# Kernel optimization log

Measured on AMD Instinct MI355X. Metric: run time of the kernel, lower is better.

The kernel has to match this reference:

```python
import jax, jax.numpy as jnp
import numpy as np

N = 100_000          # total nodes across batch
E = 3_200_000        # total edges
L = 64               # token sequence length per node
VOCAB = 6
EMBED = 16
HID = 16             # gcn_hidden
EDGE_FEAT = 5
EDGE_HID = 16
NUM_GRAPHS = 64
NODE_IN = EMBED + 1  # Hseq concat x_cov


def setup_inputs() -> dict:
    key = jax.random.key(0)
    ks = jax.random.split(key, 14)
    seq_tokens = jax.random.randint(ks[0], (N, L), 0, VOCAB, dtype=jnp.int32)
    x_cov = jax.random.normal(ks[1], (N, 1), dtype=jnp.float32)
    edge_index = jax.random.randint(ks[2], (2, E), 0, N, dtype=jnp.int32)
    edge_attr = jax.random.normal(ks[3], (E, EDGE_FEAT), dtype=jnp.float32)
    batch = jnp.sort(jax.random.randint(ks[4], (N,), 0, NUM_GRAPHS, dtype=jnp.int32))
    # parameters
    embed = jax.random.normal(ks[5], (VOCAB, EMBED), dtype=jnp.float32) * 0.1
    embed = embed.at[0].set(0.0)  # padding_idx=0
    w1 = jax.random.normal(ks[6], (NODE_IN, HID), dtype=jnp.float32) * (NODE_IN ** -0.5)
    b1 = jnp.zeros((HID,), jnp.float32)
    w2 = jax.random.normal(ks[7], (HID, HID), dtype=jnp.float32) * (HID ** -0.5)
    b2 = jnp.zeros((HID,), jnp.float32)
    we1 = jax.random.normal(ks[8], (2 * HID + EDGE_FEAT, EDGE_HID), dtype=jnp.float32) * ((2 * HID + EDGE_FEAT) ** -0.5)
    be1 = jnp.zeros((EDGE_HID,), jnp.float32)
    we2 = jax.random.normal(ks[9], (EDGE_HID, 1), dtype=jnp.float32) * (EDGE_HID ** -0.5)
    be2 = jnp.zeros((1,), jnp.float32)
    return dict(seq_tokens=seq_tokens, x_cov=x_cov, edge_index=edge_index,
                edge_attr=edge_attr, batch=batch, embed=embed,
                w1=w1, b1=b1, w2=w2, b2=b2, we1=we1, be1=be1, we2=we2, be2=be2)


def reference(seq_tokens, x_cov, edge_index, edge_attr, batch,
              embed, w1, b1, w2, b2, we1, be1, we2, be2):
    # --- encode_nodes: masked mean of token embeddings + covariate ---
    Emb = embed[seq_tokens]                                   # [N, L, EMBED]
    mask = (seq_tokens != 0).astype(jnp.float32)[..., None]   # [N, L, 1]
    lengths = jnp.maximum(mask.sum(axis=1), 1.0)              # [N, 1]
    Hseq = (Emb * mask).sum(axis=1) / lengths                 # [N, EMBED]
    X = jnp.concatenate([Hseq, x_cov], axis=1)                # [N, NODE_IN]

    # --- per-graph dense GCN, expressed as equivalent block-diagonal sparse MP ---
    src, dst = edge_index[0], edge_index[1]
    valid = (batch[src] == batch[dst]).astype(jnp.float32)    # within-graph edges only
    # row-sum degree: out-degree (valid edges) + self loop + eps, per torch code
    deg = jax.ops.segment_sum(valid, src, num_segments=N) + 1.0 + 1e-8
    dinv = deg ** -0.5                                        # [N]

    def gcn(H, W, b):
        M = H @ W + b                                         # [N, HID]
        msg = (valid * dinv[dst])[:, None] * M[dst]           # [E, HID]
        agg = jax.ops.segment_sum(msg, src, num_segments=N)   # scatter-add over src
        return jax.nn.relu(dinv[:, None] * (agg + dinv[:, None] * M))

    H = gcn(X, w1, b1)
    H = gcn(H, w2, b2)

    # --- edge MLP on gathered node pairs ---
    feats = jnp.concatenate([H[src], H[dst], edge_attr], axis=1)  # [E, 2*HID+5]
    h = jax.nn.relu(feats @ we1 + be1)
    logits = (h @ we2 + be2)[:, 0]                            # [E]
    return logits
```

## Files before the change

kernel.cpp:

```cpp
#include <hip/hip_runtime.h>
#include <hip/hip_bf16.h>
#include <hip/hip_fp16.h>

#define BS 256
#define BS3 256
#define NG 64
#define NMAX 2048
#define SEGCAP 4096
#define SUBN 16
#define SUBCAP 256

__device__ __forceinline__ uint4 pack8(const float* f) {
    union { uint4 u; __half2 h[4]; } v;
    v.h[0] = __floats2half2_rn(f[0], f[1]);
    v.h[1] = __floats2half2_rn(f[2], f[3]);
    v.h[2] = __floats2half2_rn(f[4], f[5]);
    v.h[3] = __floats2half2_rn(f[6], f[7]);
    return v.u;
}

__device__ __forceinline__ void unpack8(uint4 u, float* f) {
    const __half2* h = (const __half2*)&u;
    float2 t;
    t = __half22float2(h[0]); f[0] = t.x; f[1] = t.y;
    t = __half22float2(h[1]); f[2] = t.x; f[3] = t.y;
    t = __half22float2(h[2]); f[4] = t.x; f[5] = t.y;
    t = __half22float2(h[3]); f[6] = t.x; f[7] = t.y;
}

__global__ __launch_bounds__(BS) void encode_kernel(
        const int* __restrict__ seq,
        const float* __restrict__ xcov,
        const int* __restrict__ batch,
        const float* __restrict__ embed,
        const float* __restrict__ w1,
        const float* __restrict__ b1,
        float* __restrict__ M1,
        int* __restrict__ gcnt,
        int* __restrict__ bnd, int N) {
    __shared__ float sE[96];
    __shared__ float sW1[272];
    __shared__ float sB1[16];
    int tid = threadIdx.x;
    for (int i = tid; i < 96; i += BS) sE[i] = embed[i];
    for (int i = tid; i < 272; i += BS) sW1[i] = w1[i];
    if (tid < 16) sB1[tid] = b1[tid];
    __syncthreads();

    if (blockIdx.x == 0) {
        for (int i = tid; i < NG * 16; i += BS) gcnt[i] = 0;
    }

    int n = blockIdx.x * BS + tid;
    if (n >= N) return;

    int b = batch[n];
    if (n == 0) {
        for (int g = 0; g <= b; g++) bnd[g] = 0;
    } else {
        int pb = batch[n - 1];
        for (int g = pb + 1; g <= b; g++) bnd[g] = n;
    }
    if (n == N - 1) {
        for (int g = b + 1; g <= NG; g++) bnd[g] = N;
    }

    const int4* t4 = (const int4*)(seq + (size_t)n * 64);
    int c1 = 0, c2 = 0, c3 = 0, c4 = 0, c5 = 0;
#pragma unroll
    for (int i = 0; i < 16; i++) {
        int4 v = t4[i];
        c1 += (v.x == 1) + (v.y == 1) + (v.z == 1) + (v.w == 1);
        c2 += (v.x == 2) + (v.y == 2) + (v.z == 2) + (v.w == 2);
        c3 += (v.x == 3) + (v.y == 3) + (v.z == 3) + (v.w == 3);
        c4 += (v.x == 4) + (v.y == 4) + (v.z == 4) + (v.w == 4);
        c5 += (v.x == 5) + (v.y == 5) + (v.z == 5) + (v.w == 5);
    }
    float f1 = (float)c1, f2 = (float)c2, f3 = (float)c3, f4 = (float)c4, f5 = (float)c5;
    float tot = f1 + f2 + f3 + f4 + f5;
    float inv = 1.0f / fmaxf(tot, 1.0f);
    float h[16];
#pragma unroll
    for (int j = 0; j < 16; j++)
        h[j] = (f1 * sE[16 + j] + f2 * sE[32 + j] + f3 * sE[48 + j] +
                f4 * sE[64 + j] + f5 * sE[80 + j]) * inv;
    float xc = xcov[n];
    float o[16];
#pragma unroll
    for (int j = 0; j < 16; j++) o[j] = sB1[j] + xc * sW1[256 + j];
#pragma unroll
    for (int k = 0; k < 16; k++) {
        float hk = h[k];
#pragma unroll
        for (int j = 0; j < 16; j++) o[j] += hk * sW1[k * 16 + j];
    }
    float4* mr = (float4*)(M1 + (size_t)n * 16);
    mr[0] = make_float4(o[0], o[1], o[2], o[3]);
    mr[1] = make_float4(o[4], o[5], o[6], o[7]);
    mr[2] = make_float4(o[8], o[9], o[10], o[11]);
    mr[3] = make_float4(o[12], o[13], o[14], o[15]);
}

__device__ __forceinline__ int find_graph(const int* bnd, int s) {
    int g = 0;
#pragma unroll
    for (int step = 32; step; step >>= 1) {
        int c = g + step;
        if (c <= NG - 1 && bnd[c] <= s) g = c;
    }
    return g;
}

__global__ __launch_bounds__(BS) void prep_kernel(
        const int* __restrict__ ei,
        const int* __restrict__ bndg,
        int2* __restrict__ glist,
        int* __restrict__ gcnt, int E) {
    __shared__ int sBnd[NG + 1];
    int tid = threadIdx.x;
    if (tid <= NG) sBnd[tid] = bndg[tid];
    __syncthreads();

    int sub = blockIdx.x & (SUBN - 1);
    int idx = (blockIdx.x * BS + tid) * 4;
    if (idx + 3 < E) {
        int4 s4 = *(const int4*)(ei + idx);
        int4 d4 = *(const int4*)(ei + E + idx);
#pragma unroll
        for (int j = 0; j < 4; j++) {
            int s = (&s4.x)[j], d = (&d4.x)[j];
            int g = find_graph(sBnd, s);
            if (d >= sBnd[g] && d < sBnd[g + 1]) {
                int pos = atomicAdd(&gcnt[g * 16 + sub], 1);
                if (pos < SUBCAP)
                    glist[(size_t)g * SEGCAP + sub * SUBCAP + pos] = make_int2(s, d);
            }
        }
    } else {
        for (int j = 0; j < 4; j++) {
            int e = idx + j;
            if (e < E) {
                int s = ei[e], d = ei[E + e];
                int g = find_graph(sBnd, s);
                if (d >= sBnd[g] && d < sBnd[g + 1]) {
                    int pos = atomicAdd(&gcnt[g * 16 + sub], 1);
                    if (pos < SUBCAP)
                        glist[(size_t)g * SEGCAP + sub * SUBCAP + pos] = make_int2(s, d);
                }
            }
        }
    }
}

__global__ __launch_bounds__(BS3) void csr_kernel(
        const int2* __restrict__ glist,
        const int* __restrict__ gcnt,
        const int* __restrict__ bnd,
        int2* __restrict__ OD,
        float* __restrict__ Dinv,
        int* __restrict__ csrD) {
    __shared__ int hist[NMAX];
    __shared__ int off[NMAX + 1];
    __shared__ int cur[NMAX];
    __shared__ int wsum[4];
    __shared__ int sCnt[SUBN];

    int tid = threadIdx.x;
    int g = blockIdx.x;
    int lo = bnd[g], hi = bnd[g + 1];
    int ng = hi - lo;
    if (ng > NMAX) ng = NMAX;

    for (int i = tid; i < NMAX; i += BS3) hist[i] = 0;
    if (tid < SUBN) {
        int c = gcnt[g * 16 + tid];
        sCnt[tid] = (c > SUBCAP) ? SUBCAP : c;
    }
    __syncthreads();

    if (ng <= 0) return;

    const int2* seg = glist + (size_t)g * SEGCAP;

    for (int idx = tid; idx < SUBN * SUBCAP; idx += BS3) {
        int c = idx >> 8;
        int k = idx & (SUBCAP - 1);
        if (k < sCnt[c]) atomicAdd(&hist[seg[c * SUBCAP + k].x - lo], 1);
    }
    __syncthreads();

    int i0 = tid * 8;
    int lv[8];
    int s = 0;
#pragma unroll
    for (int k = 0; k < 8; k++) { lv[k] = hist[i0 + k]; s += lv[k]; }
    int lane = tid & 63, wv = tid >> 6;
    int x = s;
#pragma unroll
    for (int o = 1; o < 64; o <<= 1) {
        int y = __shfl_up(x, o);
        if (lane >= o) x += y;
    }
    if (lane == 63) wsum[wv] = x;
    __syncthreads();
    if (wv == 0 && lane < 4) {
        int w = wsum[lane];
#pragma unroll
        for (int o = 1; o < 4; o <<= 1) {
            int y = __shfl_up(w, o);
            if (lane >= o) w += y;
        }
        wsum[lane] = w;
    }
    __syncthreads();
    int base = (wv > 0) ? wsum[wv - 1] : 0;
    int excl = base + x - s;
    int run = excl;
#pragma unroll
    for (int k = 0; k < 8; k++) {
        off[i0 + k] = run;
        cur[i0 + k] = run;
        run += lv[k];
    }
    __syncthreads();

    int gbase = g * SEGCAP;
    for (int i = tid; i < ng; i += BS3) {
        int beg = off[i];
        int dg = ((i + 1 < NMAX) ? off[i + 1] : beg) - beg;
        OD[lo + i] = make_int2(gbase + beg, dg);
        float dgf = (float)dg + 1.0f + 1e-8f;
        Dinv[lo + i] = 1.0f / sqrtf(dgf);
    }

    for (int idx = tid; idx < SUBN * SUBCAP; idx += BS3) {
        int c = idx >> 8;
        int k = idx & (SUBCAP - 1);
        if (k < sCnt[c]) {
            int2 e = seg[c * SUBCAP + k];
            int pos = atomicAdd(&cur[e.x - lo], 1);
            csrD[gbase + pos] = e.y;
        }
    }
}

__global__ __launch_bounds__(BS) void layer1_kernel(
        const int2* __restrict__ OD,
        const float* __restrict__ Dinv,
        const int* __restrict__ csrD,
        const float* __restrict__ M1,
        float* __restrict__ M2,
        const float* __restrict__ w2,
        const float* __restrict__ b2,
        int N) {
    __shared__ float sW2[256];
    __shared__ float sB2[16];
    int tid = threadIdx.x;
    for (int i = tid; i < 256; i += BS) sW2[i] = w2[i];
    if (tid < 16) sB2[tid] = b2[tid];
    __syncthreads();

    int n = blockIdx.x * BS + tid;
    if (n >= N) return;

    int2 od = OD[n];
    float di = Dinv[n];
    float acc[16];
#pragma unroll
    for (int j = 0; j < 16; j++) acc[j] = 0.f;
    int end = od.x + od.y;
    for (int e = od.x; e < end; e++) {
        int d = csrD[e];
        float dd = Dinv[d];
        const float4* m4 = (const float4*)(M1 + (size_t)d * 16);
        float4 a = m4[0], b = m4[1], c = m4[2], q = m4[3];
        acc[0] += dd * a.x; acc[1] += dd * a.y; acc[2] += dd * a.z; acc[3] += dd * a.w;
        acc[4] += dd * b.x; acc[5] += dd * b.y; acc[6] += dd * b.z; acc[7] += dd * b.w;
        acc[8] += dd * c.x; acc[9] += dd * c.y; acc[10] += dd * c.z; acc[11] += dd * c.w;
        acc[12] += dd * q.x; acc[13] += dd * q.y; acc[14] += dd * q.z; acc[15] += dd * q.w;
    }
    const float4* mr = (const float4*)(M1 + (size_t)n * 16);
    float4 m0 = mr[0], m1 = mr[1], m2 = mr[2], m3 = mr[3];
    float m[16] = {m0.x,m0.y,m0.z,m0.w, m1.x,m1.y,m1.z,m1.w,
                   m2.x,m2.y,m2.z,m2.w, m3.x,m3.y,m3.z,m3.w};
    float h[16];
#pragma unroll
    for (int j = 0; j < 16; j++) h[j] = fmaxf(di * (acc[j] + di * m[j]), 0.0f);
    float o[16];
#pragma unroll
    for (int j = 0; j < 16; j++) o[j] = sB2[j];
#pragma unroll
    for (int k = 0; k < 16; k++) {
        float hk = h[k];
#pragma unroll
        for (int j = 0; j < 16; j++) o[j] += hk * sW2[k * 16 + j];
    }
    float4* wr = (float4*)(M2 + (size_t)n * 16);
    wr[0] = make_float4(o[0], o[1], o[2], o[3]);
    wr[1] = make_float4(o[4], o[5], o[6], o[7]);
    wr[2] = make_float4(o[8], o[9], o[10], o[11]);
    wr[3] = make_float4(o[12], o[13], o[14], o[15]);
}

__global__ __launch_bounds__(BS) void layer2_kernel(
        const int2* __restrict__ OD,
        const float* __restrict__ Dinv,
        const int* __restrict__ csrD,
        const float* __restrict__ M2,
        char* __restrict__ PQ,
        const float* __restrict__ we1,
        int N) {
    __shared__ float sWe1[512];
    int tid = threadIdx.x;
    for (int i = tid; i < 512; i += BS) sWe1[i] = we1[i];
    __syncthreads();

    int n = blockIdx.x * BS + tid;
    if (n >= N) return;

    int2 od = OD[n];
    float di = Dinv[n];
    float acc[16];
#pragma unroll
    for (int j = 0; j < 16; j++) acc[j] = 0.f;
    int end = od.x + od.y;
    for (int e = od.x; e < end; e++) {
        int d = csrD[e];
        float dd = Dinv[d];
        const float4* m4 = (const float4*)(M2 + (size_t)d * 16);
        float4 a = m4[0], b = m4[1], c = m4[2], q = m4[3];
        acc[0] += dd * a.x; acc[1] += dd * a.y; acc[2] += dd * a.z; acc[3] += dd * a.w;
        acc[4] += dd * b.x; acc[5] += dd * b.y; acc[6] += dd * b.z; acc[7] += dd * b.w;
        acc[8] += dd * c.x; acc[9] += dd * c.y; acc[10] += dd * c.z; acc[11] += dd * c.w;
        acc[12] += dd * q.x; acc[13] += dd * q.y; acc[14] += dd * q.z; acc[15] += dd * q.w;
    }
    const float4* mr = (const float4*)(M2 + (size_t)n * 16);
    float4 m0 = mr[0], m1 = mr[1], m2 = mr[2], m3 = mr[3];
    float m[16] = {m0.x,m0.y,m0.z,m0.w, m1.x,m1.y,m1.z,m1.w,
                   m2.x,m2.y,m2.z,m2.w, m3.x,m3.y,m3.z,m3.w};
    float h[16];
#pragma unroll
    for (int j = 0; j < 16; j++) h[j] = fmaxf(di * (acc[j] + di * m[j]), 0.0f);
    float p[16], q[16];
#pragma unroll
    for (int j = 0; j < 16; j++) { p[j] = 0.f; q[j] = 0.f; }
#pragma unroll
    for (int k = 0; k < 16; k++) {
        float hk = h[k];
#pragma unroll
        for (int j = 0; j < 16; j++) {
            p[j] += hk * sWe1[k * 16 + j];
            q[j] += hk * sWe1[(16 + k) * 16 + j];
        }
    }
    uint4* pr = (uint4*)(PQ + (size_t)n * 64);
    pr[0] = pack8(p); pr[1] = pack8(p + 8);
    pr[2] = pack8(q); pr[3] = pack8(q + 8);
}

__global__ __launch_bounds__(BS) void edge_mlp_kernel(
        const int* __restrict__ ei,
        const char* __restrict__ PQ,
        const float* __restrict__ eattr,
        const float* __restrict__ we1,
        const float* __restrict__ be1,
        const float* __restrict__ we2,
        const float* __restrict__ be2,
        float* __restrict__ out, int E) {
    __shared__ float sC[80];
    __shared__ float sB[16];
    __shared__ float sV[16];
    __shared__ float sb2;
    int tid = threadIdx.x;
    if (tid < 80) sC[tid] = we1[512 + tid];
    if (tid < 16) { sB[tid] = be1[tid]; sV[tid] = we2[tid]; }
    if (tid == 0) sb2 = be2[0];
    __syncthreads();
    int e = blockIdx.x * BS + tid;
    if (e >= E) return;
    int s = __builtin_nontemporal_load(ei + e);
    int d = __builtin_nontemporal_load(ei + E + e);
    const uint4* pr = (const uint4*)(PQ + (size_t)s * 64);
    const uint4* qr = (const uint4*)(PQ + (size_t)d * 64 + 32);
    uint4 pa = pr[0], pb = pr[1];
    uint4 qa = qr[0], qb = qr[1];
    const float* ea = eattr + (size_t)e * 5;
    float a0 = __builtin_nontemporal_load(ea + 0);
    float a1 = __builtin_nontemporal_load(ea + 1);
    float a2 = __builtin_nontemporal_load(ea + 2);
    float a3 = __builtin_nontemporal_load(ea + 3);
    float a4 = __builtin_nontemporal_load(ea + 4);

    float p[16], q[16];
    unpack8(pa, p); unpack8(pb, p + 8);
    unpack8(qa, q); unpack8(qb, q + 8);

    float lg = sb2;
#pragma unroll
    for (int j = 0; j < 16; j++) {
        float acc = sB[j] + p[j] + q[j] +
                    a0 * sC[j] + a1 * sC[16 + j] + a2 * sC[32 + j] +
                    a3 * sC[48 + j] + a4 * sC[64 + j];
        lg += fmaxf(acc, 0.0f) * sV[j];
    }
    __builtin_nontemporal_store(lg, out + e);
}

extern "C" void kernel_launch(void* const* d_in, const int* in_sizes, int n_in,
                              void* d_out, int out_size, void* d_ws, size_t ws_size,
                              hipStream_t stream) {
    const int* seq     = (const int*)d_in[0];
    const float* xcov  = (const float*)d_in[1];
    const int* ei      = (const int*)d_in[2];
    const float* eattr = (const float*)d_in[3];
    const int* batch   = (const int*)d_in[4];
    const float* embed = (const float*)d_in[5];
    const float* w1    = (const float*)d_in[6];
    const float* b1    = (const float*)d_in[7];
    const float* w2    = (const float*)d_in[8];
    const float* b2    = (const float*)d_in[9];
    const float* we1   = (const float*)d_in[10];
    const float* be1   = (const float*)d_in[11];
    const float* we2   = (const float*)d_in[12];
    const float* be2   = (const float*)d_in[13];
    float* out         = (float*)d_out;

    int N = in_sizes[1];
    int E = in_sizes[2] / 2;

    char* ws = (char*)d_ws;
    size_t off = 0;
    auto alloc = [&](size_t bytes) -> void* {
        void* p = ws + off;
        off += (bytes + 255) & ~(size_t)255;
        return p;
    };
    float* M1    = (float*)alloc((size_t)N * 16 * sizeof(float));
    float* M2    = (float*)alloc((size_t)N * 16 * sizeof(float));
    char* PQ     = (char*)alloc((size_t)N * 64);
    int* bndg    = (int*)alloc((NG + 1) * sizeof(int));
    int* gcnt    = (int*)alloc(NG * 16 * sizeof(int));
    int2* glist  = (int2*)alloc((size_t)NG * SEGCAP * sizeof(int2));
    int2* OD     = (int2*)alloc((size_t)N * sizeof(int2));
    float* Dinv  = (float*)alloc((size_t)N * sizeof(float));
    int* csrD    = (int*)alloc((size_t)NG * SEGCAP * sizeof(int));

    int gn = (N + BS - 1) / BS;
    int gp = (E + BS * 4 - 1) / (BS * 4);
    int ge = (E + BS - 1) / BS;

    encode_kernel<<<gn, BS, 0, stream>>>(seq, xcov, batch, embed, w1, b1,
                                         M1, gcnt, bndg, N);
    prep_kernel<<<gp, BS, 0, stream>>>(ei, bndg, glist, gcnt, E);
    csr_kernel<<<NG, BS3, 0, stream>>>(glist, gcnt, bndg, OD, Dinv, csrD);
    layer1_kernel<<<gn, BS, 0, stream>>>(OD, Dinv, csrD, M1, M2, w2, b2, N);
    layer2_kernel<<<gn, BS, 0, stream>>>(OD, Dinv, csrD, M2, PQ, we1, N);
    edge_mlp_kernel<<<ge, BS, 0, stream>>>(ei, PQ, eattr, we1, be1, we2, be2, out, E);
}
```

Measured before the change: 270.9 us.

## Replace per-graph CSR build with global degree scan and compact edge list

```diff
diff --git a/kernel.cpp b/kernel.cpp
--- a/kernel.cpp
+++ b/kernel.cpp
@@ -3,12 +3,9 @@
 #include <hip/hip_fp16.h>
 
 #define BS 256
-#define BS3 256
 #define NG 64
-#define NMAX 2048
-#define SEGCAP 4096
-#define SUBN 16
-#define SUBCAP 256
+#define VCAP 131072
+#define PBUF 256
 
 __device__ __forceinline__ uint4 pack8(const float* f) {
     union { uint4 u; __half2 h[4]; } v;
@@ -36,69 +33,70 @@
         const float* __restrict__ w1,
         const float* __restrict__ b1,
         float* __restrict__ M1,
-        int* __restrict__ gcnt,
+        int* __restrict__ deg,
+        int* __restrict__ tail,
         int* __restrict__ bnd, int N) {
     __shared__ float sE[96];
     __shared__ float sW1[272];
     __shared__ float sB1[16];
+    __shared__ float sEW[80];
     int tid = threadIdx.x;
     for (int i = tid; i < 96; i += BS) sE[i] = embed[i];
     for (int i = tid; i < 272; i += BS) sW1[i] = w1[i];
     if (tid < 16) sB1[tid] = b1[tid];
     __syncthreads();
-
-    if (blockIdx.x == 0) {
-        for (int i = tid; i < NG * 16; i += BS) gcnt[i] = 0;
-    }
-
-    int n = blockIdx.x * BS + tid;
+    if (tid < 80) {
+        int t = tid >> 4, j = tid & 15;
+        float a = 0.f;
+#pragma unroll
+        for (int k = 0; k < 16; k++) a += sE[(t + 1) * 16 + k] * sW1[k * 16 + j];
+        sEW[tid] = a;
+    }
+    __syncthreads();
+
+    int gid = blockIdx.x * BS + tid;
+    if (gid < N) deg[gid] = 0;
+    if (gid == 0) *tail = 0;
+
+    int n = blockIdx.x * 16 + (tid >> 4);
+    int j = tid & 15;
     if (n >= N) return;
 
-    int b = batch[n];
-    if (n == 0) {
-        for (int g = 0; g <= b; g++) bnd[g] = 0;
-    } else {
-        int pb = batch[n - 1];
-        for (int g = pb + 1; g <= b; g++) bnd[g] = n;
-    }
-    if (n == N - 1) {
-        for (int g = b + 1; g <= NG; g++) bnd[g] = N;
-    }
-
-    const int4* t4 = (const int4*)(seq + (size_t)n * 64);
-    int c1 = 0, c2 = 0, c3 = 0, c4 = 0, c5 = 0;
-#pragma unroll
-    for (int i = 0; i < 16; i++) {
-        int4 v = t4[i];
-        c1 += (v.x == 1) + (v.y == 1) + (v.z == 1) + (v.w == 1);
-        c2 += (v.x == 2) + (v.y == 2) + (v.z == 2) + (v.w == 2);
-        c3 += (v.x == 3) + (v.y == 3) + (v.z == 3) + (v.w == 3);
-        c4 += (v.x == 4) + (v.y == 4) + (v.z == 4) + (v.w == 4);
-        c5 += (v.x == 5) + (v.y == 5) + (v.z == 5) + (v.w == 5);
+    if (j == 0) {
+        int b = batch[n];
+        if (n == 0) {
+            for (int g = 0; g <= b; g++) bnd[g] = 0;
+        } else {
+            int pb = batch[n - 1];
+            for (int g = pb + 1; g <= b; g++) bnd[g] = n;
+        }
+        if (n == N - 1) {
+            for (int g = b + 1; g <= NG; g++) bnd[g] = N;
+        }
+    }
+
+    int4 v = ((const int4*)seq)[(size_t)n * 16 + j];
+    int c1 = (v.x == 1) + (v.y == 1) + (v.z == 1) + (v.w == 1);
+    int c2 = (v.x == 2) + (v.y == 2) + (v.z == 2) + (v.w == 2);
+    int c3 = (v.x == 3) + (v.y == 3) + (v.z == 3) + (v.w == 3);
+    int c4 = (v.x == 4) + (v.y == 4) + (v.z == 4) + (v.w == 4);
+    int c5 = (v.x == 5) + (v.y == 5) + (v.z == 5) + (v.w == 5);
+#pragma unroll
+    for (int m = 1; m < 16; m <<= 1) {
+        c1 += __shfl_xor(c1, m);
+        c2 += __shfl_xor(c2, m);
+        c3 += __shfl_xor(c3, m);
+        c4 += __shfl_xor(c4, m);
+        c5 += __shfl_xor(c5, m);
     }
     float f1 = (float)c1, f2 = (float)c2, f3 = (float)c3, f4 = (float)c4, f5 = (float)c5;
     float tot = f1 + f2 + f3 + f4 + f5;
     float inv = 1.0f / fmaxf(tot, 1.0f);
-    float h[16];
-#pragma unroll
-    for (int j = 0; j < 16; j++)
-        h[j] = (f1 * sE[16 + j] + f2 * sE[32 + j] + f3 * sE[48 + j] +
-                f4 * sE[64 + j] + f5 * sE[80 + j]) * inv;
     float xc = xcov[n];
-    float o[16];
-#pragma unroll
-    for (int j = 0; j < 16; j++) o[j] = sB1[j] + xc * sW1[256 + j];
-#pragma unroll
-    for (int k = 0; k < 16; k++) {
-        float hk = h[k];
-#pragma unroll
-        for (int j = 0; j < 16; j++) o[j] += hk * sW1[k * 16 + j];
-    }
-    float4* mr = (float4*)(M1 + (size_t)n * 16);
-    mr[0] = make_float4(o[0], o[1], o[2], o[3]);
-    mr[1] = make_float4(o[4], o[5], o[6], o[7]);
-    mr[2] = make_float4(o[8], o[9], o[10], o[11]);
-    mr[3] = make_float4(o[12], o[13], o[14], o[15]);
+    float o = sB1[j] + xc * sW1[256 + j] +
+              inv * (f1 * sEW[j] + f2 * sEW[16 + j] + f3 * sEW[32 + j] +
+                     f4 * sEW[48 + j] + f5 * sEW[64 + j]);
+    M1[(size_t)n * 16 + j] = o;
 }
 
 __device__ __forceinline__ int find_graph(const int* bnd, int s) {
@@ -114,14 +112,18 @@
 __global__ __launch_bounds__(BS) void prep_kernel(
         const int* __restrict__ ei,
         const int* __restrict__ bndg,
-        int2* __restrict__ glist,
-        int* __restrict__ gcnt, int E) {
+        int* __restrict__ deg,
+        int2* __restrict__ vlist,
+        int* __restrict__ tail, int E) {
     __shared__ int sBnd[NG + 1];
+    __shared__ int2 sList[PBUF];
+    __shared__ int sCnt;
+    __shared__ int sBase;
     int tid = threadIdx.x;
     if (tid <= NG) sBnd[tid] = bndg[tid];
-    __syncthreads();
-
-    int sub = blockIdx.x & (SUBN - 1);
+    if (tid == 0) sCnt = 0;
+    __syncthreads();
+
     int idx = (blockIdx.x * BS + tid) * 4;
     if (idx + 3 < E) {
         int4 s4 = *(const int4*)(ei + idx);
@@ -131,9 +133,9 @@
             int s = (&s4.x)[j], d = (&d4.x)[j];
             int g = find_graph(sBnd, s);
             if (d >= sBnd[g] && d < sBnd[g + 1]) {
-                int pos = atomicAdd(&gcnt[g * 16 + sub], 1);
-                if (pos < SUBCAP)
-                    glist[(size_t)g * SEGCAP + sub * SUBCAP + pos] = make_int2(s, d);
+                atomicAdd(&deg[s], 1);
+                int lp = atomicAdd(&sCnt, 1);
+                if (lp < PBUF) sList[lp] = make_int2(s, d);
             }
         }
     } else {
@@ -143,59 +145,42 @@
                 int s = ei[e], d = ei[E + e];
                 int g = find_graph(sBnd, s);
                 if (d >= sBnd[g] && d < sBnd[g + 1]) {
-                    int pos = atomicAdd(&gcnt[g * 16 + sub], 1);
-                    if (pos < SUBCAP)
-                        glist[(size_t)g * SEGCAP + sub * SUBCAP + pos] = make_int2(s, d);
+                    atomicAdd(&deg[s], 1);
+                    int lp = atomicAdd(&sCnt, 1);
+                    if (lp < PBUF) sList[lp] = make_int2(s, d);
                 }
             }
         }
     }
-}
-
-__global__ __launch_bounds__(BS3) void csr_kernel(
-        const int2* __restrict__ glist,
-        const int* __restrict__ gcnt,
-        const int* __restrict__ bnd,
-        int2* __restrict__ OD,
-        float* __restrict__ Dinv,
-        int* __restrict__ csrD) {
-    __shared__ int hist[NMAX];
-    __shared__ int off[NMAX + 1];
-    __shared__ int cur[NMAX];
+    __syncthreads();
+    if (tid == 0) {
+        int c = sCnt < PBUF ? sCnt : PBUF;
+        sBase = atomicAdd(tail, c);
+        sCnt = c;
+    }
+    __syncthreads();
+    int c = sCnt, b = sBase;
+    for (int i = tid; i < c; i += BS) {
+        int gp = b + i;
+        if (gp < VCAP) vlist[gp] = sList[i];
+    }
+}
+
+__global__ __launch_bounds__(BS) void scan1_kernel(
+        const int* __restrict__ deg,
+        int* __restrict__ off,
+        int* __restrict__ bsum,
+        int* __restrict__ csrD, int N) {
     __shared__ int wsum[4];
-    __shared__ int sCnt[SUBN];
-
     int tid = threadIdx.x;
-    int g = blockIdx.x;
-    int lo = bnd[g], hi = bnd[g + 1];
-    int ng = hi - lo;
-    if (ng > NMAX) ng = NMAX;
-
-    for (int i = tid; i < NMAX; i += BS3) hist[i] = 0;
-    if (tid < SUBN) {
-        int c = gcnt[g * 16 + tid];
-        sCnt[tid] = (c > SUBCAP) ? SUBCAP : c;
-    }
-    __syncthreads();
-
-    if (ng <= 0) return;
-
-    const int2* seg = glist + (size_t)g * SEGCAP;
-
-    for (int idx = tid; idx < SUBN * SUBCAP; idx += BS3) {
-        int c = idx >> 8;
-        int k = idx & (SUBCAP - 1);
-        if (k < sCnt[c]) atomicAdd(&hist[seg[c * SUBCAP + k].x - lo], 1);
-    }
-    __syncthreads();
-
-    int i0 = tid * 8;
-    int lv[8];
-    int s = 0;
-#pragma unroll
-    for (int k = 0; k < 8; k++) { lv[k] = hist[i0 + k]; s += lv[k]; }
+    int n = blockIdx.x * BS + tid;
+
+    int stride = gridDim.x * BS;
+    for (int i = blockIdx.x * BS + tid; i < VCAP; i += stride) csrD[i] = 0;
+
+    int v = (n < N) ? deg[n] : 0;
     int lane = tid & 63, wv = tid >> 6;
-    int x = s;
+    int x = v;
 #pragma unroll
     for (int o = 1; o < 64; o <<= 1) {
         int y = __shfl_up(x, o);
@@ -214,33 +199,64 @@
     }
     __syncthreads();
     int base = (wv > 0) ? wsum[wv - 1] : 0;
-    int excl = base + x - s;
-    int run = excl;
+    if (n < N) off[n] = base + x - v;
+    if (tid == BS - 1) bsum[blockIdx.x] = wsum[3];
+}
+
+__global__ __launch_bounds__(64) void scan2_kernel(int* __restrict__ bsum, int nb) {
+    int lane = threadIdx.x;
+    int l[8];
+    int s = 0;
+    int base0 = lane * 8;
 #pragma unroll
     for (int k = 0; k < 8; k++) {
-        off[i0 + k] = run;
-        cur[i0 + k] = run;
-        run += lv[k];
-    }
-    __syncthreads();
-
-    int gbase = g * SEGCAP;
-    for (int i = tid; i < ng; i += BS3) {
-        int beg = off[i];
-        int dg = ((i + 1 < NMAX) ? off[i + 1] : beg) - beg;
-        OD[lo + i] = make_int2(gbase + beg, dg);
-        float dgf = (float)dg + 1.0f + 1e-8f;
-        Dinv[lo + i] = 1.0f / sqrtf(dgf);
-    }
-
-    for (int idx = tid; idx < SUBN * SUBCAP; idx += BS3) {
-        int c = idx >> 8;
-        int k = idx & (SUBCAP - 1);
-        if (k < sCnt[c]) {
-            int2 e = seg[c * SUBCAP + k];
-            int pos = atomicAdd(&cur[e.x - lo], 1);
-            csrD[gbase + pos] = e.y;
-        }
+        int i = base0 + k;
+        l[k] = (i < nb) ? bsum[i] : 0;
+        s += l[k];
+    }
+    int x = s;
+#pragma unroll
+    for (int o = 1; o < 64; o <<= 1) {
+        int y = __shfl_up(x, o);
+        if (lane >= o) x += y;
+    }
+    int run = x - s;
+#pragma unroll
+    for (int k = 0; k < 8; k++) {
+        int i = base0 + k;
+        if (i < nb) bsum[i] = run;
+        run += l[k];
+    }
+}
+
+__global__ __launch_bounds__(BS) void scan3_kernel(
+        const int* __restrict__ deg,
+        const int* __restrict__ off,
+        const int* __restrict__ bsum,
+        int2* __restrict__ OD,
+        int* __restrict__ cur,
+        float* __restrict__ Dinv, int N) {
+    int n = blockIdx.x * BS + threadIdx.x;
+    if (n >= N) return;
+    int beg = off[n] + bsum[blockIdx.x];
+    int dg = deg[n];
+    OD[n] = make_int2(beg, dg);
+    cur[n] = beg;
+    Dinv[n] = 1.0f / sqrtf((float)dg + 1.0f + 1e-8f);
+}
+
+__global__ __launch_bounds__(BS) void place_kernel(
+        const int2* __restrict__ vlist,
+        const int* __restrict__ tail,
+        int* __restrict__ cur,
+        int* __restrict__ csrD) {
+    int nt = *tail;
+    if (nt > VCAP) nt = VCAP;
+    int stride = gridDim.x * BS;
+    for (int i = blockIdx.x * BS + threadIdx.x; i < nt; i += stride) {
+        int2 e = vlist[i];
+        int pos = atomicAdd(&cur[e.x], 1);
+        if (pos < VCAP) csrD[pos] = e.y;
     }
 }
 
@@ -268,8 +284,10 @@
     float acc[16];
 #pragma unroll
     for (int j = 0; j < 16; j++) acc[j] = 0.f;
-    int end = od.x + od.y;
-    for (int e = od.x; e < end; e++) {
+    int beg = od.x, end = od.x + od.y;
+    if (beg > VCAP) beg = VCAP;
+    if (end > VCAP) end = VCAP;
+    for (int e = beg; e < end; e++) {
         int d = csrD[e];
         float dd = Dinv[d];
         const float4* m4 = (const float4*)(M1 + (size_t)d * 16);
@@ -323,8 +341,10 @@
     float acc[16];
 #pragma unroll
     for (int j = 0; j < 16; j++) acc[j] = 0.f;
-    int end = od.x + od.y;
-    for (int e = od.x; e < end; e++) {
+    int beg = od.x, end = od.x + od.y;
+    if (beg > VCAP) beg = VCAP;
+    if (end > VCAP) end = VCAP;
+    for (int e = beg; e < end; e++) {
         int d = csrD[e];
         float dd = Dinv[d];
         const float4* m4 = (const float4*)(M2 + (size_t)d * 16);
@@ -356,6 +376,24 @@
     uint4* pr = (uint4*)(PQ + (size_t)n * 64);
     pr[0] = pack8(p); pr[1] = pack8(p + 8);
     pr[2] = pack8(q); pr[3] = pack8(q + 8);
+}
+
+__device__ __forceinline__ float mlp_one(
+        uint4 pa, uint4 pb, uint4 qa, uint4 qb,
+        float a0, float a1, float a2, float a3, float a4,
+        const float* sB, const float* sC, const float* sV, float sb2) {
+    float p[16], q[16];
+    unpack8(pa, p); unpack8(pb, p + 8);
+    unpack8(qa, q); unpack8(qb, q + 8);
+    float lg = sb2;
+#pragma unroll
+    for (int j = 0; j < 16; j++) {
+        float acc = sB[j] + p[j] + q[j] +
+                    a0 * sC[j] + a1 * sC[16 + j] + a2 * sC[32 + j] +
+                    a3 * sC[48 + j] + a4 * sC[64 + j];
+        lg += fmaxf(acc, 0.0f) * sV[j];
+    }
+    return lg;
 }
 
 __global__ __launch_bounds__(BS) void edge_mlp_kernel(
@@ -376,34 +414,48 @@
     if (tid < 16) { sB[tid] = be1[tid]; sV[tid] = we2[tid]; }
     if (tid == 0) sb2 = be2[0];
     __syncthreads();
-    int e = blockIdx.x * BS + tid;
-    if (e >= E) return;
-    int s = __builtin_nontemporal_load(ei + e);
-    int d = __builtin_nontemporal_load(ei + E + e);
-    const uint4* pr = (const uint4*)(PQ + (size_t)s * 64);
-    const uint4* qr = (const uint4*)(PQ + (size_t)d * 64 + 32);
-    uint4 pa = pr[0], pb = pr[1];
-    uint4 qa = qr[0], qb = qr[1];
-    const float* ea = eattr + (size_t)e * 5;
-    float a0 = __builtin_nontemporal_load(ea + 0);
-    float a1 = __builtin_nontemporal_load(ea + 1);
-    float a2 = __builtin_nontemporal_load(ea + 2);
-    float a3 = __builtin_nontemporal_load(ea + 3);
-    float a4 = __builtin_nontemporal_load(ea + 4);
-
-    float p[16], q[16];
-    unpack8(pa, p); unpack8(pb, p + 8);
-    unpack8(qa, q); unpack8(qb, q + 8);
-
-    float lg = sb2;
-#pragma unroll
-    for (int j = 0; j < 16; j++) {
-        float acc = sB[j] + p[j] + q[j] +
-                    a0 * sC[j] + a1 * sC[16 + j] + a2 * sC[32 + j] +
-                    a3 * sC[48 + j] + a4 * sC[64 + j];
-        lg += fmaxf(acc, 0.0f) * sV[j];
-    }
-    __builtin_nontemporal_store(lg, out + e);
+
+    int e0 = (blockIdx.x * BS + tid) * 4;
+    if (e0 >= E) return;
+
+    if (e0 + 3 < E) {
+        int4 s4 = *(const int4*)(ei + e0);
+        int4 d4 = *(const int4*)(ei + E + e0);
+        const uint4* p0 = (const uint4*)(PQ + (size_t)s4.x * 64);
+        const uint4* p1 = (const uint4*)(PQ + (size_t)s4.y * 64);
+        const uint4* p2 = (const uint4*)(PQ + (size_t)s4.z * 64);
+        const uint4* p3 = (const uint4*)(PQ + (size_t)s4.w * 64);
+        const uint4* q0 = (const uint4*)(PQ + (size_t)d4.x * 64 + 32);
+        const uint4* q1 = (const uint4*)(PQ + (size_t)d4.y * 64 + 32);
+        const uint4* q2 = (const uint4*)(PQ + (size_t)d4.z * 64 + 32);
+        const uint4* q3 = (const uint4*)(PQ + (size_t)d4.w * 64 + 32);
+        uint4 pa0 = p0[0], pb0 = p0[1], qa0 = q0[0], qb0 = q0[1];
+        uint4 pa1 = p1[0], pb1 = p1[1], qa1 = q1[0], qb1 = q1[1];
+        uint4 pa2 = p2[0], pb2 = p2[1], qa2 = q2[0], qb2 = q2[1];
+        uint4 pa3 = p3[0], pb3 = p3[1], qa3 = q3[0], qb3 = q3[1];
+        const float4* at = (const float4*)(eattr + (size_t)e0 * 5);
+        float4 A0 = at[0], A1 = at[1], A2 = at[2], A3 = at[3], A4 = at[4];
+
+        float r0 = mlp_one(pa0, pb0, qa0, qb0, A0.x, A0.y, A0.z, A0.w, A1.x, sB, sC, sV, sb2);
+        float r1 = mlp_one(pa1, pb1, qa1, qb1, A1.y, A1.z, A1.w, A2.x, A2.y, sB, sC, sV, sb2);
+        float r2 = mlp_one(pa2, pb2, qa2, qb2, A2.z, A2.w, A3.x, A3.y, A3.z, sB, sC, sV, sb2);
+        float r3 = mlp_one(pa3, pb3, qa3, qb3, A3.w, A4.x, A4.y, A4.z, A4.w, sB, sC, sV, sb2);
+        *(float4*)(out + e0) = make_float4(r0, r1, r2, r3);
+    } else {
+        for (int j = 0; j < 4; j++) {
+            int e = e0 + j;
+            if (e < E) {
+                int s = ei[e], d = ei[E + e];
+                const uint4* pr = (const uint4*)(PQ + (size_t)s * 64);
+                const uint4* qr = (const uint4*)(PQ + (size_t)d * 64 + 32);
+                uint4 pa = pr[0], pb = pr[1], qa = qr[0], qb = qr[1];
+                const float* ea = eattr + (size_t)e * 5;
+                float lg = mlp_one(pa, pb, qa, qb, ea[0], ea[1], ea[2], ea[3], ea[4],
+                                   sB, sC, sV, sb2);
+                out[e] = lg;
+            }
+        }
+    }
 }
 
 extern "C" void kernel_launch(void* const* d_in, const int* in_sizes, int n_in,
@@ -429,31 +481,39 @@
     int E = in_sizes[2] / 2;
 
     char* ws = (char*)d_ws;
-    size_t off = 0;
+    size_t off_b = 0;
     auto alloc = [&](size_t bytes) -> void* {
-        void* p = ws + off;
-        off += (bytes + 255) & ~(size_t)255;
+        void* p = ws + off_b;
+        off_b += (bytes + 255) & ~(size_t)255;
         return p;
     };
     float* M1    = (float*)alloc((size_t)N * 16 * sizeof(float));
     float* M2    = (float*)alloc((size_t)N * 16 * sizeof(float));
     char* PQ     = (char*)alloc((size_t)N * 64);
     int* bndg    = (int*)alloc((NG + 1) * sizeof(int));
-    int* gcnt    = (int*)alloc(NG * 16 * sizeof(int));
-    int2* glist  = (int2*)alloc((size_t)NG * SEGCAP * sizeof(int2));
+    int* deg     = (int*)alloc((size_t)N * sizeof(int));
+    int* offA    = (int*)alloc((size_t)N * sizeof(int));
+    int* cur     = (int*)alloc((size_t)N * sizeof(int));
     int2* OD     = (int2*)alloc((size_t)N * sizeof(int2));
     float* Dinv  = (float*)alloc((size_t)N * sizeof(float));
-    int* csrD    = (int*)alloc((size_t)NG * SEGCAP * sizeof(int));
-
-    int gn = (N + BS - 1) / BS;
-    int gp = (E + BS * 4 - 1) / (BS * 4);
-    int ge = (E + BS - 1) / BS;
-
-    encode_kernel<<<gn, BS, 0, stream>>>(seq, xcov, batch, embed, w1, b1,
-                                         M1, gcnt, bndg, N);
-    prep_kernel<<<gp, BS, 0, stream>>>(ei, bndg, glist, gcnt, E);
-    csr_kernel<<<NG, BS3, 0, stream>>>(glist, gcnt, bndg, OD, Dinv, csrD);
-    layer1_kernel<<<gn, BS, 0, stream>>>(OD, Dinv, csrD, M1, M2, w2, b2, N);
-    layer2_kernel<<<gn, BS, 0, stream>>>(OD, Dinv, csrD, M2, PQ, we1, N);
-    edge_mlp_kernel<<<ge, BS, 0, stream>>>(ei, PQ, eattr, we1, be1, we2, be2, out, E);
-}
+    int* bsum    = (int*)alloc(512 * sizeof(int));
+    int2* vlist  = (int2*)alloc((size_t)VCAP * sizeof(int2));
+    int* csrD    = (int*)alloc((size_t)VCAP * sizeof(int));
+    int* tail    = (int*)alloc(16 * sizeof(int));
+
+    int gn16 = ((size_t)N * 16 + BS - 1) / BS;
+    int gp   = (E + BS * 4 - 1) / (BS * 4);
+    int gs   = (N + BS - 1) / BS;
+    int ge4  = (E + BS * 4 - 1) / (BS * 4);
+
+    encode_kernel<<<gn16, BS, 0, stream>>>(seq, xcov, batch, embed, w1, b1,
+                                           M1, deg, tail, bndg, N);
+    prep_kernel<<<gp, BS, 0, stream>>>(ei, bndg, deg, vlist, tail, E);
+    scan1_kernel<<<gs, BS, 0, stream>>>(deg, offA, bsum, csrD, N);
+    scan2_kernel<<<1, 64, 0, stream>>>(bsum, gs);
+    scan3_kernel<<<gs, BS, 0, stream>>>(deg, offA, bsum, OD, cur, Dinv, N);
+    place_kernel<<<208, BS, 0, stream>>>(vlist, tail, cur, csrD);
+    layer1_kernel<<<gs, BS, 0, stream>>>(OD, Dinv, csrD, M1, M2, w2, b2, N);
+    layer2_kernel<<<gs, BS, 0, stream>>>(OD, Dinv, csrD, M2, PQ, we1, N);
+    edge_mlp_kernel<<<ge4, BS, 0, stream>>>(ei, PQ, eattr, we1, be1, we2, be2, out, E);
+}
```

Result: slower. 301.3 us (+11.2%).
